# Optimization experiments

Measured on AMD Instinct MI355X. Metric: run time of the kernel, lower is better.

## Reference

```python
import jax, jax.numpy as jnp
import numpy as np
import math

B, S, E, H = 2, 2048, 1024, 16
D = E // H  # head_dim = 64


def setup_inputs() -> dict:
    key = jax.random.key(0)
    ks = jax.random.split(key, 12)
    scale = 1.0 / math.sqrt(E)
    inp = {
        "q": jax.random.normal(ks[0], (B, S, E), jnp.float32),
        "k": jax.random.normal(ks[1], (B, S, E), jnp.float32),
        "v": jax.random.normal(ks[2], (B, S, E), jnp.float32),
        # causal mask, broadcast over batch and heads
        "mask": jnp.tril(jnp.ones((S, S), jnp.bool_))[None, None, :, :],
        "Wq": jax.random.normal(ks[3], (E, E), jnp.float32) * scale,
        "bq": jnp.zeros((E,), jnp.float32),
        "Wk": jax.random.normal(ks[4], (E, E), jnp.float32) * scale,
        "bk": jnp.zeros((E,), jnp.float32),
        "Wv": jax.random.normal(ks[5], (E, E), jnp.float32) * scale,
        "bv": jnp.zeros((E,), jnp.float32),
        "Wo": jax.random.normal(ks[6], (E, E), jnp.float32) * scale,
        "bo": jnp.zeros((E,), jnp.float32),
    }
    return inp


def _heads(x, W, b):
    # nn.Linear: x @ W.T + b, then split into heads -> [B, H, S, D]
    y = x @ W.T + b
    return y.reshape(B, S, H, D).transpose(0, 2, 1, 3)


def reference(q, k, v, mask, Wq, bq, Wk, bk, Wv, bv, Wo, bo):
    qh = _heads(q, Wq, bq)   # [B,H,S,D]
    kh = _heads(k, Wk, bk)
    vh = _heads(v, Wv, bv)
    scores = jnp.einsum("bhqd,bhkd->bhqk", qh, kh) / math.sqrt(D)
    scores = jnp.where(mask, scores, -1e9)
    probs = jax.nn.softmax(scores, axis=-1)  # dropout is identity in eval
    ctx = jnp.einsum("bhqk,bhkd->bhqd", probs, vh)
    ctx = ctx.transpose(0, 2, 1, 3).reshape(B, S, E)
    return ctx @ Wo.T + bo
```

## Files before the change

### kernel.cpp

```cpp
#include <hip/hip_runtime.h>
#include <hip/hip_bf16.h>
#include <cstdint>

#define PB 2
#define PS 2048
#define PE 1024
#define PH 16
#define PD 64

typedef __attribute__((ext_vector_type(8))) short short8;
typedef __attribute__((ext_vector_type(8))) ushort u16x8;
typedef __attribute__((ext_vector_type(4))) float f32x4;

static __device__ __forceinline__ float bf2f(ushort u) {
  return __uint_as_float(((unsigned)u) << 16);
}
static __device__ __forceinline__ ushort f2bf(float f) {
  unsigned u = __float_as_uint(f);
  u += 0x7fffu + ((u >> 16) & 1u);
  return (ushort)(u >> 16);
}
static __device__ __forceinline__ unsigned pkbf(float a, float b) {
  __hip_bfloat162 h = __float22bfloat162_rn(make_float2(a, b));
  return *reinterpret_cast<unsigned*>(&h);
}
static __device__ __forceinline__ u16x8 cvt8(f32x4 a, f32x4 b) {
  union { unsigned u[4]; u16x8 v; } r;
  r.u[0] = pkbf(a[0], a[1]); r.u[1] = pkbf(a[2], a[3]);
  r.u[2] = pkbf(b[0], b[1]); r.u[3] = pkbf(b[2], b[3]);
  return r.v;
}

static __device__ __forceinline__ void async16(void* lds, const void* g) {
  __attribute__((address_space(3))) unsigned* l =
      reinterpret_cast<__attribute__((address_space(3))) unsigned*>(
          reinterpret_cast<uintptr_t>(lds));
  const __attribute__((address_space(1))) unsigned* gp =
      reinterpret_cast<const __attribute__((address_space(1))) unsigned*>(
          reinterpret_cast<uintptr_t>(g));
  __builtin_amdgcn_global_load_lds(gp, l, 16, 0, 0);
}

__global__ __launch_bounds__(256)
void cvt_kernel(const float* __restrict__ s0, const float* __restrict__ s1,
                const float* __restrict__ s2, const float* __restrict__ s3,
                const float* __restrict__ s4, const float* __restrict__ s5,
                const float* __restrict__ s6,
                ushort* d0, ushort* d1, ushort* d2, ushort* d3, ushort* d4,
                ushort* d5, ushort* d6) {
  const int t = blockIdx.y;
  const float* src = t == 0 ? s0 : t == 1 ? s1 : t == 2 ? s2 : t == 3 ? s3
                   : t == 4 ? s4 : t == 5 ? s5 : s6;
  ushort* dst = t == 0 ? d0 : t == 1 ? d1 : t == 2 ? d2 : t == 3 ? d3
              : t == 4 ? d4 : t == 5 ? d5 : d6;
  const size_t n = (t < 3) ? (size_t)4194304 : (size_t)1048576;
  const size_t i0 = ((size_t)blockIdx.x * 256 + threadIdx.x) * 16;
  if (i0 >= n) return;
  const f32x4 a = *(const f32x4*)(src + i0);
  const f32x4 b = *(const f32x4*)(src + i0 + 4);
  const f32x4 c = *(const f32x4*)(src + i0 + 8);
  const f32x4 d = *(const f32x4*)(src + i0 + 12);
  *(u16x8*)(dst + i0) = cvt8(a, b);
  *(u16x8*)(dst + i0 + 8) = cvt8(c, d);
}

template <bool SWAP>
__device__ __forceinline__ void gemm_core(const ushort* __restrict__ A,
                                          const ushort* __restrict__ W,
                                          int m0, int n0,
                                          ushort* As, ushort* Bs,
                                          f32x4 acc[4][4]) {
  const int tid  = threadIdx.x;
  const int wave = tid >> 6;
  const int lane = tid & 63;
  const int quad = lane >> 4;
  const int lrow = lane & 15;
  const int wm = wave >> 1;
  const int wn = wave & 1;
  const int row0 = tid >> 2;
  const int kc8  = (tid & 3) * 8;

  auto stage = [&](int buf, int kt) {
    ushort* Ab = As + buf * 4096;
    ushort* Bb = Bs + buf * 4096;
    async16(Ab + (size_t)wave * 512,        A + (size_t)(m0 + row0)      * PE + kt + kc8);
    async16(Ab + 2048 + (size_t)wave * 512, A + (size_t)(m0 + row0 + 64) * PE + kt + kc8);
    async16(Bb + (size_t)wave * 512,        W + (size_t)(n0 + row0)      * PE + kt + kc8);
    async16(Bb + 2048 + (size_t)wave * 512, W + (size_t)(n0 + row0 + 64) * PE + kt + kc8);
  };

  stage(0, 0);
  __syncthreads();
  int cur = 0;

  for (int kt = 0; kt < PE; kt += 32) {
    if (kt + 32 < PE) stage(cur ^ 1, kt + 32);
    const ushort* Ab = As + cur * 4096;
    const ushort* Bb = Bs + cur * 4096;
    short8 af[4], bf[4];
#pragma unroll
    for (int i = 0; i < 4; ++i) {
      af[i] = *(const short8*)(Ab + (wm * 64 + i * 16 + lrow) * 32 + quad * 8);
      bf[i] = *(const short8*)(Bb + (wn * 64 + i * 16 + lrow) * 32 + quad * 8);
    }
#pragma unroll
    for (int i = 0; i < 4; ++i)
#pragma unroll
      for (int j = 0; j < 4; ++j) {
        if (SWAP)
          acc[i][j] = __builtin_amdgcn_mfma_f32_16x16x32_bf16(bf[j], af[i], acc[i][j], 0, 0, 0);
        else
          acc[i][j] = __builtin_amdgcn_mfma_f32_16x16x32_bf16(af[i], bf[j], acc[i][j], 0, 0, 0);
      }
    __syncthreads();
    cur ^= 1;
  }
}

__global__ __launch_bounds__(256)
void qkv_kernel(const ushort* __restrict__ q, const ushort* __restrict__ k,
                const ushort* __restrict__ v,
                const ushort* __restrict__ Wq, const ushort* __restrict__ Wk,
                const ushort* __restrict__ Wv,
                const float* __restrict__ bq, const float* __restrict__ bk,
                const float* __restrict__ bv,
                ushort* __restrict__ qh, ushort* __restrict__ kh,
                ushort* __restrict__ vt) {
  __shared__ __align__(16) ushort As[2 * 128 * 32];
  __shared__ __align__(16) ushort Bs[2 * 128 * 32];
  const int which = blockIdx.y >> 3;
  const int n0 = (blockIdx.y & 7) * 128;
  const int m0 = blockIdx.x * 128;
  const ushort* A  = which == 0 ? q  : (which == 1 ? k  : v);
  const ushort* W  = which == 0 ? Wq : (which == 1 ? Wk : Wv);
  const float* bi  = which == 0 ? bq : (which == 1 ? bk : bv);

  const int lane = threadIdx.x & 63;
  const int wave = threadIdx.x >> 6;
  const int quad = lane >> 4, lrow = lane & 15;
  const int wm = wave >> 1, wn = wave & 1;

  f32x4 acc[4][4] = {};
  if (which == 2) {
    gemm_core<true>(A, W, m0, n0, As, Bs, acc);
#pragma unroll
    for (int j = 0; j < 4; ++j) {
#pragma unroll
      for (int i = 0; i < 4; ++i) {
        const int xrow = m0 + wm * 64 + i * 16 + lrow;
        const int b = xrow >> 11, s = xrow & 2047;
#pragma unroll
        for (int r = 0; r < 4; ++r) {
          const int dcol = n0 + wn * 64 + j * 16 + quad * 4 + r;
          const int h = dcol >> 6, d = dcol & 63;
          vt[((size_t)((b << 4) + h) << 17) + ((size_t)d << 11) + s] =
              f2bf(acc[i][j][r] + bi[dcol]);
        }
      }
    }
  } else {
    gemm_core<false>(A, W, m0, n0, As, Bs, acc);
    ushort* Out = which == 0 ? qh : kh;
#pragma unroll
    for (int j = 0; j < 4; ++j) {
      const int col = n0 + wn * 64 + j * 16 + lrow;
      const float bias = bi[col];
      const int h = col >> 6, d = col & 63;
#pragma unroll
      for (int i = 0; i < 4; ++i)
#pragma unroll
        for (int r = 0; r < 4; ++r) {
          const int row = m0 + wm * 64 + i * 16 + quad * 4 + r;
          const int b = row >> 11, s = row & 2047;
          Out[((size_t)((b << 4) + h) << 17) + ((size_t)s << 6) + d] =
              f2bf(acc[i][j][r] + bias);
        }
    }
  }
}

__global__ __launch_bounds__(256)
void outproj_kernel(const ushort* __restrict__ ctx, const ushort* __restrict__ Wo,
                    const float* __restrict__ bo, float* __restrict__ out) {
  __shared__ __align__(16) ushort As[2 * 128 * 32];
  __shared__ __align__(16) ushort Bs[2 * 128 * 32];
  const int n0 = blockIdx.y * 128;
  const int m0 = blockIdx.x * 128;

  f32x4 acc[4][4] = {};
  gemm_core<false>(ctx, Wo, m0, n0, As, Bs, acc);

  const int lane = threadIdx.x & 63;
  const int wave = threadIdx.x >> 6;
  const int quad = lane >> 4, lrow = lane & 15;
  const int wm = wave >> 1, wn = wave & 1;
#pragma unroll
  for (int j = 0; j < 4; ++j) {
    const int col = n0 + wn * 64 + j * 16 + lrow;
    const float bias = bo[col];
#pragma unroll
    for (int i = 0; i < 4; ++i)
#pragma unroll
      for (int r = 0; r < 4; ++r) {
        const int row = m0 + wm * 64 + i * 16 + quad * 4 + r;
        out[((size_t)row << 10) + col] = acc[i][j][r] + bias;
      }
  }
}

#define SW_IDX(r, g) (((r) << 6) + ((((g) ^ ((r) & 7))) << 3))
#define QSCALE 0.180336879f
#define SOFF 24.0f

__global__ __launch_bounds__(256)
void attn_kernel(const ushort* __restrict__ qh, const ushort* __restrict__ kh,
                 const ushort* __restrict__ vt, ushort* __restrict__ ctx) {
  __shared__ __align__(16) ushort Ks[2][4096];
  __shared__ __align__(16) ushort Vs[2][4096];
  __shared__ __align__(16) ushort Ps[4][1024];
  const int tid  = threadIdx.x;
  const int wave = tid >> 6;
  const int lane = tid & 63;
  const int quad = lane >> 4;
  const int lrow = lane & 15;
  const int bh = blockIdx.x, b = bh >> 4, h = bh & 15;
  const size_t base = (size_t)bh << 17;
  const int srow = tid >> 2;
  const int sg0  = (tid & 3) * 2;
  const int pr   = wave * 16 + lrow;
  ushort* Pw = &Ps[wave][0];
  const int prow = lrow << 6;

  const int qb = 31 - blockIdx.y;
  const int q0 = qb * 64;

  short8 qf0, qf1;
  {
    const ushort* qp = qh + base + (size_t)(q0 + pr) * 64 + quad * 8;
    const u16x8 a = *(const u16x8*)qp;
    const u16x8 c = *(const u16x8*)(qp + 32);
#pragma unroll
    for (int j = 0; j < 8; ++j) {
      qf0[j] = (short)f2bf(bf2f(a[j]) * QSCALE);
      qf1[j] = (short)f2bf(bf2f(c[j]) * QSCALE);
    }
  }

  f32x4 o_acc[4] = {};
  float l_i = 0.f;

  u16x8 kst0, kst1, vst0, vst1;
  {
    const ushort* kp = kh + base + (size_t)srow * 64 + sg0 * 8;
    kst0 = *(const u16x8*)kp; kst1 = *(const u16x8*)(kp + 8);
    const ushort* vp = vt + base + (size_t)srow * 2048 + sg0 * 8;
    vst0 = *(const u16x8*)vp; vst1 = *(const u16x8*)(vp + 8);
  }

  for (int kt = 0; kt <= qb; ++kt) {
    const int buf = kt & 1;
    *(u16x8*)&Ks[buf][SW_IDX(srow, sg0)]     = kst0;
    *(u16x8*)&Ks[buf][SW_IDX(srow, sg0 + 1)] = kst1;
    *(u16x8*)&Vs[buf][SW_IDX(srow, sg0)]     = vst0;
    *(u16x8*)&Vs[buf][SW_IDX(srow, sg0 + 1)] = vst1;
    __syncthreads();

    if (kt < qb) {
      const ushort* kp = kh + base + (size_t)((kt + 1) * 64 + srow) * 64 + sg0 * 8;
      kst0 = *(const u16x8*)kp; kst1 = *(const u16x8*)(kp + 8);
      const ushort* vp = vt + base + (size_t)srow * 2048 + (kt + 1) * 64 + sg0 * 8;
      vst0 = *(const u16x8*)vp; vst1 = *(const u16x8*)(vp + 8);
    }

    f32x4 st[4] = {};
#pragma unroll
    for (int nt = 0; nt < 4; ++nt) {
      const int r = nt * 16 + lrow;
      const short8 kb0 = *(const short8*)&Ks[buf][SW_IDX(r, quad)];
      const short8 kb1 = *(const short8*)&Ks[buf][SW_IDX(r, quad + 4)];
      st[nt] = __builtin_amdgcn_mfma_f32_16x16x32_bf16(kb0, qf0, st[nt], 0, 0, 0);
      st[nt] = __builtin_amdgcn_mfma_f32_16x16x32_bf16(kb1, qf1, st[nt], 0, 0, 0);
    }

    if (kt == qb) {
#pragma unroll
      for (int nt = 0; nt < 4; ++nt)
#pragma unroll
        for (int r = 0; r < 4; ++r)
          if (nt * 16 + quad * 4 + r > pr) st[nt][r] = -1e30f;
    }

    float rs = 0.f;
#pragma unroll
    for (int nt = 0; nt < 4; ++nt) {
      float p0 = exp2f(st[nt][0] - SOFF);
      float p1 = exp2f(st[nt][1] - SOFF);
      float p2 = exp2f(st[nt][2] - SOFF);
      float p3 = exp2f(st[nt][3] - SOFF);
      rs += (p0 + p1) + (p2 + p3);
      uint2 pk;
      pk.x = pkbf(p0, p1); pk.y = pkbf(p2, p3);
      *(uint2*)&Pw[prow + (((nt * 2 + (quad >> 1)) ^ (lrow & 7)) << 3) +
                   (quad & 1) * 4] = pk;
    }
    rs += __shfl_xor(rs, 16);
    rs += __shfl_xor(rs, 32);
    l_i += rs;

    const short8 pa0 = *(const short8*)&Pw[prow + ((quad ^ (lrow & 7)) << 3)];
    const short8 pa1 = *(const short8*)&Pw[prow + (((quad + 4) ^ (lrow & 7)) << 3)];
#pragma unroll
    for (int nt = 0; nt < 4; ++nt) {
      const int r = nt * 16 + lrow;
      const short8 vb0 = *(const short8*)&Vs[buf][SW_IDX(r, quad)];
      const short8 vb1 = *(const short8*)&Vs[buf][SW_IDX(r, quad + 4)];
      o_acc[nt] = __builtin_amdgcn_mfma_f32_16x16x32_bf16(vb0, pa0, o_acc[nt], 0, 0, 0);
      o_acc[nt] = __builtin_amdgcn_mfma_f32_16x16x32_bf16(vb1, pa1, o_acc[nt], 0, 0, 0);
    }
  }

  const float inv = 1.f / l_i;
  const size_t rowb = ((size_t)b << 21) + ((size_t)(q0 + pr) << 10) + (h << 6);
#pragma unroll
  for (int nt = 0; nt < 4; ++nt) {
    uint2 u;
    u.x = pkbf(o_acc[nt][0] * inv, o_acc[nt][1] * inv);
    u.y = pkbf(o_acc[nt][2] * inv, o_acc[nt][3] * inv);
    *(uint2*)(ctx + rowb + nt * 16 + quad * 4) = u;
  }
}

extern "C" void kernel_launch(void* const* d_in, const int* in_sizes, int n_in,
                              void* d_out, int out_size, void* d_ws, size_t ws_size,
                              hipStream_t stream) {
  const float* q  = (const float*)d_in[0];
  const float* k  = (const float*)d_in[1];
  const float* v  = (const float*)d_in[2];
  const float* Wq = (const float*)d_in[4];
  const float* bq = (const float*)d_in[5];
  const float* Wk = (const float*)d_in[6];
  const float* bk = (const float*)d_in[7];
  const float* Wv = (const float*)d_in[8];
  const float* bv = (const float*)d_in[9];
  const float* Wo = (const float*)d_in[10];
  const float* bo = (const float*)d_in[11];

  const size_t NTOK = (size_t)PB * PS * PE;
  const size_t NW   = (size_t)PE * PE;
  ushort* qh  = (ushort*)d_ws;
  ushort* kh  = qh + NTOK;
  ushort* vt  = kh + NTOK;
  ushort* qc  = vt + NTOK;
  ushort* kc  = qc + NTOK;
  ushort* vc  = kc + NTOK;
  ushort* wqc = vc + NTOK;
  ushort* wkc = wqc + NW;
  ushort* wvc = wkc + NW;
  ushort* woc = wvc + NW;
  ushort* ctx = qc;

  cvt_kernel<<<dim3(1024, 7), dim3(256), 0, stream>>>(
      q, k, v, Wq, Wk, Wv, Wo, qc, kc, vc, wqc, wkc, wvc, woc);
  qkv_kernel<<<dim3(32, 24), dim3(256), 0, stream>>>(
      qc, kc, vc, wqc, wkc, wvc, bq, bk, bv, qh, kh, vt);
  attn_kernel<<<dim3(32, 32), dim3(256), 0, stream>>>(qh, kh, vt, ctx);
  outproj_kernel<<<dim3(32, 8), dim3(256), 0, stream>>>(
      ctx, woc, bo, (float*)d_out);
}
```

Before: 221.5 us.

## Pair high and low causal query tiles per block to balance work and share K/V

Each attention block now handles two query tiles, tile 31-y and tile y, so every block does the same total number of causal key tiles. The K/V tiles loaded into shared memory are reused for both query tiles, which halves K/V staging for the low tile. The softmax offset is folded into the MFMA accumulator's initial value. The grid shrinks from 1024 to 512 blocks, and register and LDS use rise, which can lower occupancy.

```diff
diff --git a/kernel.cpp b/kernel.cpp
--- a/kernel.cpp
+++ b/kernel.cpp
@@ -217,7 +217,8 @@
                  const ushort* __restrict__ vt, ushort* __restrict__ ctx) {
   __shared__ __align__(16) ushort Ks[2][4096];
   __shared__ __align__(16) ushort Vs[2][4096];
-  __shared__ __align__(16) ushort Ps[4][1024];
+  __shared__ __align__(16) ushort PsH[4][1024];
+  __shared__ __align__(16) ushort PsL[4][1024];
   const int tid  = threadIdx.x;
   const int wave = tid >> 6;
   const int lane = tid & 63;
@@ -228,26 +229,33 @@
   const int srow = tid >> 2;
   const int sg0  = (tid & 3) * 2;
   const int pr   = wave * 16 + lrow;
-  ushort* Pw = &Ps[wave][0];
+  ushort* PwH = &PsH[wave][0];
+  ushort* PwL = &PsL[wave][0];
   const int prow = lrow << 6;
 
-  const int qb = 31 - blockIdx.y;
-  const int q0 = qb * 64;
-
-  short8 qf0, qf1;
+  const int y   = blockIdx.y;
+  const int qbH = 31 - y, qbL = y;
+  const int q0H = qbH * 64, q0L = qbL * 64;
+
+  short8 qH0, qH1, qL0, qL1;
   {
-    const ushort* qp = qh + base + (size_t)(q0 + pr) * 64 + quad * 8;
-    const u16x8 a = *(const u16x8*)qp;
-    const u16x8 c = *(const u16x8*)(qp + 32);
+    const ushort* qpH = qh + base + (size_t)(q0H + pr) * 64 + quad * 8;
+    const u16x8 a = *(const u16x8*)qpH;
+    const u16x8 c = *(const u16x8*)(qpH + 32);
+    const ushort* qpL = qh + base + (size_t)(q0L + pr) * 64 + quad * 8;
+    const u16x8 a2 = *(const u16x8*)qpL;
+    const u16x8 c2 = *(const u16x8*)(qpL + 32);
 #pragma unroll
     for (int j = 0; j < 8; ++j) {
-      qf0[j] = (short)f2bf(bf2f(a[j]) * QSCALE);
-      qf1[j] = (short)f2bf(bf2f(c[j]) * QSCALE);
-    }
-  }
-
-  f32x4 o_acc[4] = {};
-  float l_i = 0.f;
+      qH0[j] = (short)f2bf(bf2f(a[j]) * QSCALE);
+      qH1[j] = (short)f2bf(bf2f(c[j]) * QSCALE);
+      qL0[j] = (short)f2bf(bf2f(a2[j]) * QSCALE);
+      qL1[j] = (short)f2bf(bf2f(c2[j]) * QSCALE);
+    }
+  }
+
+  f32x4 oH[4] = {}, oL[4] = {};
+  float lH = 0.f, lL = 0.f;
 
   u16x8 kst0, kst1, vst0, vst1;
   {
@@ -257,7 +265,7 @@
     vst0 = *(const u16x8*)vp; vst1 = *(const u16x8*)(vp + 8);
   }
 
-  for (int kt = 0; kt <= qb; ++kt) {
+  for (int kt = 0; kt <= qbH; ++kt) {
     const int buf = kt & 1;
     *(u16x8*)&Ks[buf][SW_IDX(srow, sg0)]     = kst0;
     *(u16x8*)&Ks[buf][SW_IDX(srow, sg0 + 1)] = kst1;
@@ -265,68 +273,140 @@
     *(u16x8*)&Vs[buf][SW_IDX(srow, sg0 + 1)] = vst1;
     __syncthreads();
 
-    if (kt < qb) {
+    if (kt < qbH) {
       const ushort* kp = kh + base + (size_t)((kt + 1) * 64 + srow) * 64 + sg0 * 8;
       kst0 = *(const u16x8*)kp; kst1 = *(const u16x8*)(kp + 8);
       const ushort* vp = vt + base + (size_t)srow * 2048 + (kt + 1) * 64 + sg0 * 8;
       vst0 = *(const u16x8*)vp; vst1 = *(const u16x8*)(vp + 8);
     }
 
-    f32x4 st[4] = {};
+    const bool doL = (kt <= qbL);
+
+    short8 kb0[4], kb1[4];
 #pragma unroll
     for (int nt = 0; nt < 4; ++nt) {
       const int r = nt * 16 + lrow;
-      const short8 kb0 = *(const short8*)&Ks[buf][SW_IDX(r, quad)];
-      const short8 kb1 = *(const short8*)&Ks[buf][SW_IDX(r, quad + 4)];
-      st[nt] = __builtin_amdgcn_mfma_f32_16x16x32_bf16(kb0, qf0, st[nt], 0, 0, 0);
-      st[nt] = __builtin_amdgcn_mfma_f32_16x16x32_bf16(kb1, qf1, st[nt], 0, 0, 0);
-    }
-
-    if (kt == qb) {
+      kb0[nt] = *(const short8*)&Ks[buf][SW_IDX(r, quad)];
+      kb1[nt] = *(const short8*)&Ks[buf][SW_IDX(r, quad + 4)];
+    }
+
+    f32x4 stH[4], stL[4];
+#pragma unroll
+    for (int nt = 0; nt < 4; ++nt) {
+      stH[nt] = (f32x4){-SOFF, -SOFF, -SOFF, -SOFF};
+      stH[nt] = __builtin_amdgcn_mfma_f32_16x16x32_bf16(kb0[nt], qH0, stH[nt], 0, 0, 0);
+      stH[nt] = __builtin_amdgcn_mfma_f32_16x16x32_bf16(kb1[nt], qH1, stH[nt], 0, 0, 0);
+    }
+    if (doL) {
+#pragma unroll
+      for (int nt = 0; nt < 4; ++nt) {
+        stL[nt] = (f32x4){-SOFF, -SOFF, -SOFF, -SOFF};
+        stL[nt] = __builtin_amdgcn_mfma_f32_16x16x32_bf16(kb0[nt], qL0, stL[nt], 0, 0, 0);
+        stL[nt] = __builtin_amdgcn_mfma_f32_16x16x32_bf16(kb1[nt], qL1, stL[nt], 0, 0, 0);
+      }
+    }
+
+    if (kt == qbH) {
 #pragma unroll
       for (int nt = 0; nt < 4; ++nt)
 #pragma unroll
         for (int r = 0; r < 4; ++r)
-          if (nt * 16 + quad * 4 + r > pr) st[nt][r] = -1e30f;
-    }
-
-    float rs = 0.f;
-#pragma unroll
-    for (int nt = 0; nt < 4; ++nt) {
-      float p0 = exp2f(st[nt][0] - SOFF);
-      float p1 = exp2f(st[nt][1] - SOFF);
-      float p2 = exp2f(st[nt][2] - SOFF);
-      float p3 = exp2f(st[nt][3] - SOFF);
-      rs += (p0 + p1) + (p2 + p3);
-      uint2 pk;
-      pk.x = pkbf(p0, p1); pk.y = pkbf(p2, p3);
-      *(uint2*)&Pw[prow + (((nt * 2 + (quad >> 1)) ^ (lrow & 7)) << 3) +
-                   (quad & 1) * 4] = pk;
-    }
-    rs += __shfl_xor(rs, 16);
-    rs += __shfl_xor(rs, 32);
-    l_i += rs;
-
-    const short8 pa0 = *(const short8*)&Pw[prow + ((quad ^ (lrow & 7)) << 3)];
-    const short8 pa1 = *(const short8*)&Pw[prow + (((quad + 4) ^ (lrow & 7)) << 3)];
+          if (nt * 16 + quad * 4 + r > pr) stH[nt][r] = -1e30f;
+    }
+    if (kt == qbL) {
+#pragma unroll
+      for (int nt = 0; nt < 4; ++nt)
+#pragma unroll
+        for (int r = 0; r < 4; ++r)
+          if (nt * 16 + quad * 4 + r > pr) stL[nt][r] = -1e30f;
+    }
+
+    {
+      float rs = 0.f;
+#pragma unroll
+      for (int nt = 0; nt < 4; ++nt) {
+        float p0 = exp2f(stH[nt][0]);
+        float p1 = exp2f(stH[nt][1]);
+        float p2 = exp2f(stH[nt][2]);
+        float p3 = exp2f(stH[nt][3]);
+        rs += (p0 + p1) + (p2 + p3);
+        uint2 pk;
+        pk.x = pkbf(p0, p1); pk.y = pkbf(p2, p3);
+        *(uint2*)&PwH[prow + (((nt * 2 + (quad >> 1)) ^ (lrow & 7)) << 3) +
+                      (quad & 1) * 4] = pk;
+      }
+      rs += __shfl_xor(rs, 16);
+      rs += __shfl_xor(rs, 32);
+      lH += rs;
+    }
+    if (doL) {
+      float rs = 0.f;
+#pragma unroll
+      for (int nt = 0; nt < 4; ++nt) {
+        float p0 = exp2f(stL[nt][0]);
+        float p1 = exp2f(stL[nt][1]);
+        float p2 = exp2f(stL[nt][2]);
+        float p3 = exp2f(stL[nt][3]);
+        rs += (p0 + p1) + (p2 + p3);
+        uint2 pk;
+        pk.x = pkbf(p0, p1); pk.y = pkbf(p2, p3);
+        *(uint2*)&PwL[prow + (((nt * 2 + (quad >> 1)) ^ (lrow & 7)) << 3) +
+                      (quad & 1) * 4] = pk;
+      }
+      rs += __shfl_xor(rs, 16);
+      rs += __shfl_xor(rs, 32);
+      lL += rs;
+    }
+
+    short8 vb0[4], vb1[4];
 #pragma unroll
     for (int nt = 0; nt < 4; ++nt) {
       const int r = nt * 16 + lrow;
-      const short8 vb0 = *(const short8*)&Vs[buf][SW_IDX(r, quad)];
-      const short8 vb1 = *(const short8*)&Vs[buf][SW_IDX(r, quad + 4)];
-      o_acc[nt] = __builtin_amdgcn_mfma_f32_16x16x32_bf16(vb0, pa0, o_acc[nt], 0, 0, 0);
-      o_acc[nt] = __builtin_amdgcn_mfma_f32_16x16x32_bf16(vb1, pa1, o_acc[nt], 0, 0, 0);
-    }
-  }
-
-  const float inv = 1.f / l_i;
-  const size_t rowb = ((size_t)b << 21) + ((size_t)(q0 + pr) << 10) + (h << 6);
-#pragma unroll
-  for (int nt = 0; nt < 4; ++nt) {
-    uint2 u;
-    u.x = pkbf(o_acc[nt][0] * inv, o_acc[nt][1] * inv);
-    u.y = pkbf(o_acc[nt][2] * inv, o_acc[nt][3] * inv);
-    *(uint2*)(ctx + rowb + nt * 16 + quad * 4) = u;
+      vb0[nt] = *(const short8*)&Vs[buf][SW_IDX(r, quad)];
+      vb1[nt] = *(const short8*)&Vs[buf][SW_IDX(r, quad + 4)];
+    }
+
+    {
+      const short8 pa0 = *(const short8*)&PwH[prow + ((quad ^ (lrow & 7)) << 3)];
+      const short8 pa1 = *(const short8*)&PwH[prow + (((quad + 4) ^ (lrow & 7)) << 3)];
+#pragma unroll
+      for (int nt = 0; nt < 4; ++nt) {
+        oH[nt] = __builtin_amdgcn_mfma_f32_16x16x32_bf16(vb0[nt], pa0, oH[nt], 0, 0, 0);
+        oH[nt] = __builtin_amdgcn_mfma_f32_16x16x32_bf16(vb1[nt], pa1, oH[nt], 0, 0, 0);
+      }
+    }
+    if (doL) {
+      const short8 pa0 = *(const short8*)&PwL[prow + ((quad ^ (lrow & 7)) << 3)];
+      const short8 pa1 = *(const short8*)&PwL[prow + (((quad + 4) ^ (lrow & 7)) << 3)];
+#pragma unroll
+      for (int nt = 0; nt < 4; ++nt) {
+        oL[nt] = __builtin_amdgcn_mfma_f32_16x16x32_bf16(vb0[nt], pa0, oL[nt], 0, 0, 0);
+        oL[nt] = __builtin_amdgcn_mfma_f32_16x16x32_bf16(vb1[nt], pa1, oL[nt], 0, 0, 0);
+      }
+    }
+  }
+
+  {
+    const float inv = 1.f / lH;
+    const size_t rowb = ((size_t)b << 21) + ((size_t)(q0H + pr) << 10) + (h << 6);
+#pragma unroll
+    for (int nt = 0; nt < 4; ++nt) {
+      uint2 u;
+      u.x = pkbf(oH[nt][0] * inv, oH[nt][1] * inv);
+      u.y = pkbf(oH[nt][2] * inv, oH[nt][3] * inv);
+      *(uint2*)(ctx + rowb + nt * 16 + quad * 4) = u;
+    }
+  }
+  {
+    const float inv = 1.f / lL;
+    const size_t rowb = ((size_t)b << 21) + ((size_t)(q0L + pr) << 10) + (h << 6);
+#pragma unroll
+    for (int nt = 0; nt < 4; ++nt) {
+      uint2 u;
+      u.x = pkbf(oL[nt][0] * inv, oL[nt][1] * inv);
+      u.y = pkbf(oL[nt][2] * inv, oL[nt][3] * inv);
+      *(uint2*)(ctx + rowb + nt * 16 + quad * 4) = u;
+    }
   }
 }
 
@@ -363,7 +443,7 @@
       q, k, v, Wq, Wk, Wv, Wo, qc, kc, vc, wqc, wkc, wvc, woc);
   qkv_kernel<<<dim3(32, 24), dim3(256), 0, stream>>>(
       qc, kc, vc, wqc, wkc, wvc, bq, bk, bv, qh, kh, vt);
-  attn_kernel<<<dim3(32, 32), dim3(256), 0, stream>>>(qh, kh, vt, ctx);
+  attn_kernel<<<dim3(32, 16), dim3(256), 0, stream>>>(qh, kh, vt, ctx);
   outproj_kernel<<<dim3(32, 8), dim3(256), 0, stream>>>(
       ctx, woc, bo, (float*)d_out);
 }
```

New measurement: 222.7 us. About the same (+0.6%).

## Compute softmax row sums via MFMA and interleave causal block order

Applied to the files above, without the earlier changes.

Row sums of the softmax probabilities are now accumulated with an MFMA against a ones vector using the bf16-rounded P, which replaces the per-tile shuffle reductions. The SOFF offset is folded into the score accumulator's initial value, which removes a subtraction before each exp2. The query-block mapping now interleaves long and short causal rows so that heavy and light blocks are mixed across dispatch order. The GEMM B-fragment load is rewritten inline but is semantically unchanged.

```diff
diff --git a/kernel.cpp b/kernel.cpp
--- a/kernel.cpp
+++ b/kernel.cpp
@@ -101,8 +101,9 @@
 #pragma unroll
     for (int i = 0; i < 4; ++i) {
       af[i] = *(const short8*)(Ab + (wm * 64 + i * 16 + lrow) * 32 + quad * 8);
-      bf[i] = *(const short8*)(Bb + (wn * 64 + i * 16 + lrow) * 32 + quad * 8);
-    }
+      bf[i] = *(const short8*)(Bs + cur * 4096 + (wn * 64 + i * 16 + lrow) * 32 + quad * 8);
+    }
+    (void)Bb;
 #pragma unroll
     for (int i = 0; i < 4; ++i)
 #pragma unroll
@@ -231,7 +232,8 @@
   ushort* Pw = &Ps[wave][0];
   const int prow = lrow << 6;
 
-  const int qb = 31 - blockIdx.y;
+  const int y  = blockIdx.y;
+  const int qb = (y < 8) ? 31 - y : (y < 16) ? y - 8 : (y < 24) ? 39 - y : y - 16;
   const int q0 = qb * 64;
 
   short8 qf0, qf1;
@@ -246,8 +248,12 @@
     }
   }
 
+  short8 ones;
+#pragma unroll
+  for (int j = 0; j < 8; ++j) ones[j] = (short)0x3F80;
+
   f32x4 o_acc[4] = {};
-  float l_i = 0.f;
+  f32x4 lacc = {};
 
   u16x8 kst0, kst1, vst0, vst1;
   {
@@ -272,12 +278,13 @@
       vst0 = *(const u16x8*)vp; vst1 = *(const u16x8*)(vp + 8);
     }
 
-    f32x4 st[4] = {};
+    f32x4 st[4];
 #pragma unroll
     for (int nt = 0; nt < 4; ++nt) {
       const int r = nt * 16 + lrow;
       const short8 kb0 = *(const short8*)&Ks[buf][SW_IDX(r, quad)];
       const short8 kb1 = *(const short8*)&Ks[buf][SW_IDX(r, quad + 4)];
+      st[nt] = (f32x4){-SOFF, -SOFF, -SOFF, -SOFF};
       st[nt] = __builtin_amdgcn_mfma_f32_16x16x32_bf16(kb0, qf0, st[nt], 0, 0, 0);
       st[nt] = __builtin_amdgcn_mfma_f32_16x16x32_bf16(kb1, qf1, st[nt], 0, 0, 0);
     }
@@ -290,25 +297,22 @@
           if (nt * 16 + quad * 4 + r > pr) st[nt][r] = -1e30f;
     }
 
-    float rs = 0.f;
 #pragma unroll
     for (int nt = 0; nt < 4; ++nt) {
-      float p0 = exp2f(st[nt][0] - SOFF);
-      float p1 = exp2f(st[nt][1] - SOFF);
-      float p2 = exp2f(st[nt][2] - SOFF);
-      float p3 = exp2f(st[nt][3] - SOFF);
-      rs += (p0 + p1) + (p2 + p3);
+      float p0 = exp2f(st[nt][0]);
+      float p1 = exp2f(st[nt][1]);
+      float p2 = exp2f(st[nt][2]);
+      float p3 = exp2f(st[nt][3]);
       uint2 pk;
       pk.x = pkbf(p0, p1); pk.y = pkbf(p2, p3);
       *(uint2*)&Pw[prow + (((nt * 2 + (quad >> 1)) ^ (lrow & 7)) << 3) +
                    (quad & 1) * 4] = pk;
     }
-    rs += __shfl_xor(rs, 16);
-    rs += __shfl_xor(rs, 32);
-    l_i += rs;
 
     const short8 pa0 = *(const short8*)&Pw[prow + ((quad ^ (lrow & 7)) << 3)];
     const short8 pa1 = *(const short8*)&Pw[prow + (((quad + 4) ^ (lrow & 7)) << 3)];
+    lacc = __builtin_amdgcn_mfma_f32_16x16x32_bf16(ones, pa0, lacc, 0, 0, 0);
+    lacc = __builtin_amdgcn_mfma_f32_16x16x32_bf16(ones, pa1, lacc, 0, 0, 0);
 #pragma unroll
     for (int nt = 0; nt < 4; ++nt) {
       const int r = nt * 16 + lrow;
@@ -319,7 +323,7 @@
     }
   }
 
-  const float inv = 1.f / l_i;
+  const float inv = 1.f / lacc[0];
   const size_t rowb = ((size_t)b << 21) + ((size_t)(q0 + pr) << 10) + (h << 6);
 #pragma unroll
   for (int nt = 0; nt < 4; ++nt) {
```

After: 218.6 us. Within noise of the previous version (-1.3%).
